# Kernel optimization log

Measured on AMD Instinct MI355X. Metric: run time of the kernel, lower is better.

Reference implementation:

```python
import jax, jax.numpy as jnp
import numpy as np

BATCH, N_BEADS, BEAD_SIZE, N_ATOMS = 32, 16384, 16, 100000
INV_SQRT2 = 0.7071067811865476  # e3nn 'uuu' 1o x 1o -> 1e (irrep_normalization='none') cross-product scale


def _mask_arrays():
    # Deterministic bead->atom mask: bead h places count_h = (h % 16) + 1 atoms.
    counts = np.arange(N_BEADS) % BEAD_SIZE + 1
    mask = np.arange(BEAD_SIZE)[None, :] < counts[:, None]  # (n_beads, bead_size)
    slot_idx = np.nonzero(mask.ravel())[0].astype(np.int32)  # flat positions of True entries, (M,)
    bead_idx = np.repeat(np.arange(N_BEADS), counts).astype(np.int32)  # bead id per placed atom, (M,)
    return slot_idx, bead_idx


def setup_inputs() -> dict:
    slot_idx, bead_idx = _mask_arrays()
    M = slot_idx.shape[0]  # 139264
    rng = np.random.default_rng(0)
    atom_idx = rng.integers(0, N_ATOMS, size=M).astype(np.int32)  # bead2atom_idcs flattened over beads
    key = jax.random.key(0)
    kP, k1, k2, kw, ka, ks = jax.random.split(key, 6)
    return {
        'P': jax.random.normal(kP, (BATCH, N_BEADS, 3), jnp.float32),
        'p1': jax.random.normal(k1, (BATCH, N_BEADS, 3), jnp.float32),
        'p2': jax.random.normal(k2, (BATCH, N_BEADS, 3), jnp.float32),
        'weights': jax.random.normal(kw, (3, N_BEADS, BEAD_SIZE), jnp.float32),
        'angles_polar': jax.random.normal(ka, (M, 1), jnp.float32),
        'scaling': jax.random.normal(ks, (N_ATOMS, 1), jnp.float32),
        'slot_idx': jnp.asarray(slot_idx),
        'atom_idx': jnp.asarray(atom_idx),
        'bead_idx': jnp.asarray(bead_idx),
    }


def _q_mult(q1, q2):
    w1, x1, y1, z1 = jnp.moveaxis(q1, -1, 0)
    w2, x2, y2, z2 = jnp.moveaxis(q2, -1, 0)
    w = w1 * w2 - x1 * x2 - y1 * y2 - z1 * z2
    x = w1 * x2 + x1 * w2 + y1 * z2 - z1 * y2
    y = w1 * y2 + y1 * w2 + z1 * x2 - x1 * z2
    z = w1 * z2 + z1 * w2 + x1 * y2 - y1 * x2
    return jnp.stack((w, x, y, z), -1)


def _qv_mult(q, v):
    q2 = jnp.concatenate([jnp.zeros(v.shape[:-1] + (1,), v.dtype), v], -1)
    q_conj = q * jnp.asarray([1.0, -1.0, -1.0, -1.0], q.dtype)
    return _q_mult(_q_mult(q, q2), q_conj)[..., 1:]


def reference(P, p1, p2, weights, angles_polar, scaling, slot_idx, atom_idx, bead_idx):
    B = P.shape[0]
    # per-bead cross product (e3nn TensorProduct 'uuu' path)
    p12 = jnp.cross(p1, p2) * jnp.asarray(INV_SQRT2, p1.dtype)
    stacked = jnp.stack([p1, p2, p12], axis=1)                      # (B, 3, H, 3)
    rot = jnp.einsum('bihk,ihl->bhlk', stacked, weights)            # (B, H, L, 3)
    rot = rot / jnp.linalg.norm(rot, axis=-1, keepdims=True)
    rot_flat = rot.reshape(B, N_BEADS * BEAD_SIZE, 3)[:, slot_idx]  # (B, M, 3) gather via mask
    # quaternions: real = cos(theta), imag = sin(theta) * axis
    cos_a = jnp.cos(angles_polar)                                   # (M, 1)
    sin_a = jnp.sin(angles_polar)
    q = jnp.concatenate([jnp.broadcast_to(cos_a, (B,) + cos_a.shape), sin_a[None] * rot_flat], -1)  # (B, M, 4)
    v = p1[:, bead_idx]                                             # (B, M, 3) repeat_interleave by counts
    v_rot = _qv_mult(q, v)                                          # (B, M, 3)
    recon = scaling[atom_idx][None] * v_rot + P[:, bead_idx]        # (B, M, 3)
    out = jnp.zeros((B, N_ATOMS, 3), P.dtype).at[:, atom_idx].add(recon)  # scatter-add (overlaps accumulate)
    return out, rot_flat.reshape(-1, 3)
```

## Files before the change

kernel.cpp:

```cpp
#include <hip/hip_runtime.h>
#include <hip/hip_fp16.h>
#include <math.h>

#define BATCH   32
#define N_BEADS 16384
#define BEAD_SIZE 16
#define N_ATOMS 100000
#define INV_SQRT2 0.70710678118654752440f
#define SCAN_BLK 256

__global__ void __launch_bounds__(256)
zero_kernel(int* __restrict__ p, int n)
{
    int i = blockIdx.x * 256 + threadIdx.x;
    if (i < n) p[i] = 0;
}

__global__ void __launch_bounds__(256)
countrec_kernel(const int* __restrict__ atom_idx,
                const int* __restrict__ slot_idx,
                const float* __restrict__ W,
                int* __restrict__ counts,
                float4* __restrict__ rec1, int M)
{
    int m = blockIdx.x * blockDim.x + threadIdx.x;
    if (m >= M) return;
    atomicAdd(&counts[atom_idx[m]], 1);
    int slot = slot_idx[m];
    int h = slot >> 4, l = slot & 15;
    float w0 = W[(0 * N_BEADS + h) * BEAD_SIZE + l];
    float w1 = W[(1 * N_BEADS + h) * BEAD_SIZE + l];
    float w2 = W[(2 * N_BEADS + h) * BEAD_SIZE + l];
    rec1[m] = make_float4(__int_as_float(slot), w0, w1, w2);
}

__global__ void __launch_bounds__(SCAN_BLK)
scan1_kernel(const int* __restrict__ counts, int* __restrict__ off,
             int* __restrict__ bsum, int n)
{
    __shared__ int s[SCAN_BLK];
    int i = blockIdx.x * SCAN_BLK + threadIdx.x;
    int c = (i < n) ? counts[i] : 0;
    s[threadIdx.x] = c;
    __syncthreads();
    int v = c;
    for (int d = 1; d < SCAN_BLK; d <<= 1) {
        int t = (threadIdx.x >= d) ? s[threadIdx.x - d] : 0;
        __syncthreads();
        v += t;
        s[threadIdx.x] = v;
        __syncthreads();
    }
    if (i < n) off[i] = v - c;
    if (threadIdx.x == SCAN_BLK - 1) bsum[blockIdx.x] = v;
}

__global__ void __launch_bounds__(256)
scan3_kernel(int* __restrict__ off, const int* __restrict__ bsum,
             const int* __restrict__ counts,
             int* __restrict__ cursor2, float4* __restrict__ rec_a, int n)
{
    __shared__ int red[256];
    int j = blockIdx.x;
    int partial = 0;
    for (int i = threadIdx.x; i < j; i += 256) partial += bsum[i];
    red[threadIdx.x] = partial;
    __syncthreads();
    for (int d = 128; d > 0; d >>= 1) {
        if ((int)threadIdx.x < d) red[threadIdx.x] += red[threadIdx.x + d];
        __syncthreads();
    }
    int bpref = red[0];
    int i = j * 256 + threadIdx.x;
    if (i >= n) return;
    int o = off[i] + bpref;
    off[i] = o;
    cursor2[i] = 0;
    rec_a[i] = make_float4(__int_as_float(counts[i]), __int_as_float(o),
                           0.f, 0.f);
}

__global__ void __launch_bounds__(256)
fill2_kernel(const int* __restrict__ atom_idx, const int* __restrict__ off,
             const float* __restrict__ ang, const float* __restrict__ scal,
             int* __restrict__ cursor2, int* __restrict__ csr_m,
             float4* __restrict__ recM2, int M)
{
    int m = blockIdx.x * blockDim.x + threadIdx.x;
    if (m >= M) return;
    int a = atom_idx[m];
    int k = atomicAdd(&cursor2[a], 1);
    csr_m[off[a] + k] = m;
    float sa, ca;
    __sincosf(ang[m], &sa, &ca);
    recM2[m] = make_float4(2.f * ca * sa, 2.f * sa * sa, scal[a], 0.f);
}

__global__ void __launch_bounds__(256)
mcontrib_kernel(const float4* __restrict__ rec1,
                const float4* __restrict__ recM2,
                const float* __restrict__ p1,
                const float* __restrict__ p2,
                const float* __restrict__ P,
                float* __restrict__ out_rot,
                uint2* __restrict__ cM16,
                int M)
{
    int bg = blockIdx.y;
    int mbase = blockIdx.x * 256;
    int m = mbase + threadIdx.x;
    int b0 = bg * 4;
    bool act = m < M;
    int mc = act ? m : (M - 1);

    float4 r1 = rec1[mc];
    float4 r2 = recM2[mc];
    int h = __float_as_int(r1.x) >> 4;
    float A = r2.x, Bc = r2.y, s = r2.z;
    size_t hoff = (size_t)h * 3;

    __shared__ float sbuf[768];
    int nm = M - mbase; if (nm > 256) nm = 256;
    int nf = nm * 3;
    int nf4 = nf >> 2;
    int done = nf4 << 2;
    int rem = nf - done;

#pragma unroll
    for (int i = 0; i < 4; ++i) {
        int b = b0 + i;
        const size_t bb = (size_t)b * N_BEADS * 3;
        const float* p1p = p1 + bb + hoff;
        const float* p2p = p2 + bb + hoff;
        const float* Pp  = P  + bb + hoff;
        float a1x = p1p[0], a1y = p1p[1], a1z = p1p[2];
        float a2x = p2p[0], a2y = p2p[1], a2z = p2p[2];

        float cxx = (a1y * a2z - a1z * a2y) * INV_SQRT2;
        float cyy = (a1z * a2x - a1x * a2z) * INV_SQRT2;
        float czz = (a1x * a2y - a1y * a2x) * INV_SQRT2;
        float rx = r1.y * a1x + r1.z * a2x + r1.w * cxx;
        float ry = r1.y * a1y + r1.z * a2y + r1.w * cyy;
        float rz = r1.y * a1z + r1.z * a2z + r1.w * czz;
        float inv = rsqrtf(rx * rx + ry * ry + rz * rz);
        rx *= inv; ry *= inv; rz *= inv;

        __syncthreads();
        sbuf[threadIdx.x * 3 + 0] = rx;
        sbuf[threadIdx.x * 3 + 1] = ry;
        sbuf[threadIdx.x * 3 + 2] = rz;
        __syncthreads();
        {
            size_t base = ((size_t)b * M + mbase) * 3;
            float4* dst = (float4*)(out_rot + base);
            if ((base & 3) == 0) {
                if ((int)threadIdx.x < nf4)
                    dst[threadIdx.x] = ((const float4*)sbuf)[threadIdx.x];
                if ((int)threadIdx.x < rem)
                    out_rot[base + done + threadIdx.x] = sbuf[done + threadIdx.x];
            } else if (act) {
                out_rot[base + threadIdx.x * 3 + 0] = rx;
                out_rot[base + threadIdx.x * 3 + 1] = ry;
                out_rot[base + threadIdx.x * 3 + 2] = rz;
            }
        }

        float ux = ry * a1z - rz * a1y;
        float uy = rz * a1x - rx * a1z;
        float uz = rx * a1y - ry * a1x;
        float wx = ry * uz - rz * uy;
        float wy = rz * ux - rx * uz;
        float wz = rx * uy - ry * ux;
        float ox = s * (a1x + A * ux + Bc * wx) + Pp[0];
        float oy = s * (a1y + A * uy + Bc * wy) + Pp[1];
        float oz = s * (a1z + A * uz + Bc * wz) + Pp[2];

        if (act) {
            union { struct { __half2 lo, hi; } h; uint2 u; } pk;
            pk.h.lo = __floats2half2_rn(ox, oy);
            pk.h.hi = __floats2half2_rn(oz, 0.f);
            cM16[(size_t)b * M + m] = pk.u;
        }
    }
}

__global__ void __launch_bounds__(256)
sum2_kernel(const float4* __restrict__ rec_a,
            const int* __restrict__ csr_m,
            const uint2* __restrict__ cM16,
            float* __restrict__ out_atoms, int M, int abps)
{
    int beta = blockIdx.x;
    int xcd  = beta & 7;
    int j    = beta >> 3;
    int round = j / abps;
    int ablk  = j - round * abps;
    int b = xcd + 8 * round;
    int abase = ablk * 256;
    int a = abase + threadIdx.x;

    float ax = 0.f, ay = 0.f, az = 0.f;
    if (a < N_ATOMS) {
        float4 ra = rec_a[a];
        int cnt = __float_as_int(ra.x);
        int o   = __float_as_int(ra.y);
        const uint2* cb = cM16 + (size_t)b * M;
        for (int k = 0; k < cnt; ++k) {
            int m = csr_m[o + k];
            union { uint2 u; struct { __half2 lo, hi; } h; } pk;
            pk.u = cb[m];
            float2 xy = __half22float2(pk.h.lo);
            float2 zp = __half22float2(pk.h.hi);
            ax += xy.x; ay += xy.y; az += zp.x;
        }
    }
    __shared__ float sbuf[768];
    sbuf[threadIdx.x * 3 + 0] = ax;
    sbuf[threadIdx.x * 3 + 1] = ay;
    sbuf[threadIdx.x * 3 + 2] = az;
    __syncthreads();

    int na = N_ATOMS - abase; if (na > 256) na = 256;
    int nf = na * 3;
    size_t base = ((size_t)b * N_ATOMS + abase) * 3;
    int nf4 = nf >> 2;
    float4* dst = (float4*)(out_atoms + base);
    if ((int)threadIdx.x < nf4)
        dst[threadIdx.x] = ((const float4*)sbuf)[threadIdx.x];
    int done = nf4 << 2;
    int rem = nf - done;
    if ((int)threadIdx.x < rem)
        out_atoms[base + done + threadIdx.x] = sbuf[done + threadIdx.x];
}

__global__ void __launch_bounds__(256)
backmap_fallback(const float* __restrict__ P, const float* __restrict__ p1,
                 const float* __restrict__ p2, const float* __restrict__ W,
                 const float* __restrict__ ang, const float* __restrict__ scal,
                 const int* __restrict__ slot_idx, const int* __restrict__ atom_idx,
                 float* __restrict__ out_atoms, float* __restrict__ out_rot, int M)
{
    int t = blockIdx.x * blockDim.x + threadIdx.x;
    if (t >= BATCH * M) return;
    int b = t / M; int m = t - b * M;
    int slot = slot_idx[m]; int h = slot >> 4; int l = slot & 15;
    int atom = atom_idx[m];
    const float* p1p = p1 + ((size_t)b * N_BEADS + h) * 3;
    const float* p2p = p2 + ((size_t)b * N_BEADS + h) * 3;
    float a1x = p1p[0], a1y = p1p[1], a1z = p1p[2];
    float a2x = p2p[0], a2y = p2p[1], a2z = p2p[2];
    float cx = (a1y * a2z - a1z * a2y) * INV_SQRT2;
    float cy = (a1z * a2x - a1x * a2z) * INV_SQRT2;
    float cz = (a1x * a2y - a1y * a2x) * INV_SQRT2;
    float w0 = W[(0 * N_BEADS + h) * BEAD_SIZE + l];
    float w1 = W[(1 * N_BEADS + h) * BEAD_SIZE + l];
    float w2 = W[(2 * N_BEADS + h) * BEAD_SIZE + l];
    float rx = w0 * a1x + w1 * a2x + w2 * cx;
    float ry = w0 * a1y + w1 * a2y + w2 * cy;
    float rz = w0 * a1z + w1 * a2z + w2 * cz;
    float inv = rsqrtf(rx * rx + ry * ry + rz * rz);
    rx *= inv; ry *= inv; rz *= inv;
    float* ro = out_rot + (size_t)t * 3;
    ro[0] = rx; ro[1] = ry; ro[2] = rz;
    float sa, ca; __sincosf(ang[m], &sa, &ca);
    float A = 2.f * ca * sa, Bc = 2.f * sa * sa;
    float ux = ry * a1z - rz * a1y;
    float uy = rz * a1x - rx * a1z;
    float uz = rx * a1y - ry * a1x;
    float wx = ry * uz - rz * uy;
    float wy = rz * ux - rx * uz;
    float wz = rx * uy - ry * ux;
    float s = scal[atom];
    const float* Pp = P + ((size_t)b * N_BEADS + h) * 3;
    float* op = out_atoms + ((size_t)b * N_ATOMS + atom) * 3;
    atomicAdd(op + 0, s * (a1x + A * ux + Bc * wx) + Pp[0]);
    atomicAdd(op + 1, s * (a1y + A * uy + Bc * wy) + Pp[1]);
    atomicAdd(op + 2, s * (a1z + A * uz + Bc * wz) + Pp[2]);
}

extern "C" void kernel_launch(void* const* d_in, const int* in_sizes, int n_in,
                              void* d_out, int out_size, void* d_ws, size_t ws_size,
                              hipStream_t stream) {
    const float* P    = (const float*)d_in[0];
    const float* p1   = (const float*)d_in[1];
    const float* p2   = (const float*)d_in[2];
    const float* W    = (const float*)d_in[3];
    const float* ang  = (const float*)d_in[4];
    const float* scal = (const float*)d_in[5];
    const int* slot_idx = (const int*)d_in[6];
    const int* atom_idx = (const int*)d_in[7];

    int M = in_sizes[6];
    float* out_atoms = (float*)d_out;
    float* out_rot   = out_atoms + (size_t)BATCH * N_ATOMS * 3;

    int nblk   = (N_ATOMS + SCAN_BLK - 1) / SCAN_BLK;
    int nchunk = (M + 255) / 256;

    size_t intpre = (size_t)N_ATOMS * 4 * 3 + 512 * 4;
    size_t need   = intpre + (size_t)M * 16 * 2 + (size_t)N_ATOMS * 16
                  + (size_t)M * 4 + (size_t)BATCH * M * 8;

    if (ws_size >= need) {
        int* counts  = (int*)d_ws;
        int* off     = counts + N_ATOMS;
        int* cursor2 = off + N_ATOMS;
        int* bsum    = cursor2 + N_ATOMS;
        float4* rec1  = (float4*)((char*)d_ws + intpre);
        float4* recM2 = rec1 + M;
        float4* rec_a = recM2 + M;
        int*    csr_m = (int*)(rec_a + N_ATOMS);
        uint2*  cM16  = (uint2*)(csr_m + M);

        zero_kernel<<<nblk, 256, 0, stream>>>(counts, N_ATOMS);
        countrec_kernel<<<nchunk, 256, 0, stream>>>(
            atom_idx, slot_idx, W, counts, rec1, M);
        scan1_kernel<<<nblk, SCAN_BLK, 0, stream>>>(counts, off, bsum, N_ATOMS);
        scan3_kernel<<<nblk, 256, 0, stream>>>(off, bsum, counts,
                                               cursor2, rec_a, N_ATOMS);
        fill2_kernel<<<nchunk, 256, 0, stream>>>(
            atom_idx, off, ang, scal, cursor2, csr_m, recM2, M);

        dim3 gm(nchunk, 8);
        mcontrib_kernel<<<gm, 256, 0, stream>>>(
            rec1, recM2, p1, p2, P, out_rot, cM16, M);

        int abps = (N_ATOMS + 255) / 256;
        sum2_kernel<<<abps * BATCH, 256, 0, stream>>>(
            rec_a, csr_m, cM16, out_atoms, M, abps);
        return;
    }

    hipMemsetAsync(out_atoms, 0, (size_t)BATCH * N_ATOMS * 3 * sizeof(float), stream);
    int total = BATCH * M;
    backmap_fallback<<<(total + 255) / 256, 256, 0, stream>>>(
        P, p1, p2, W, ang, scal, slot_idx, atom_idx,
        out_atoms, out_rot, M);
}
```

Before: 91.72 us.

## Stage per-block bead vectors in LDS and batch rotation stores after compute

The mcontrib kernel now loads each block's contiguous range of bead vectors (p1, p2, P for four batches) into shared memory with cooperative coalesced reads, replacing repeated strided per-thread global loads. It falls back to global loads if a bead lies outside the staged range. The rot outputs for all four batches are buffered in shared memory, so the two barriers per batch iteration are replaced by one barrier and a final coalesced store pass. This uses more shared memory and adds a staging barrier, which may reduce occupancy.

```diff
diff --git a/kernel.cpp b/kernel.cpp
--- a/kernel.cpp
+++ b/kernel.cpp
@@ -8,6 +8,7 @@
 #define N_ATOMS 100000
 #define INV_SQRT2 0.70710678118654752440f
 #define SCAN_BLK 256
+#define NH 64
 
 __global__ void __launch_bounds__(256)
 zero_kernel(int* __restrict__ p, int n)
@@ -108,7 +109,8 @@
 {
     int bg = blockIdx.y;
     int mbase = blockIdx.x * 256;
-    int m = mbase + threadIdx.x;
+    int tid = threadIdx.x;
+    int m = mbase + tid;
     int b0 = bg * 4;
     bool act = m < M;
     int mc = act ? m : (M - 1);
@@ -117,24 +119,49 @@
     float4 r2 = recM2[mc];
     int h = __float_as_int(r1.x) >> 4;
     float A = r2.x, Bc = r2.y, s = r2.z;
-    size_t hoff = (size_t)h * 3;
-
-    __shared__ float sbuf[768];
-    int nm = M - mbase; if (nm > 256) nm = 256;
-    int nf = nm * 3;
-    int nf4 = nf >> 2;
-    int done = nf4 << 2;
-    int rem = nf - done;
+
+    __shared__ float sbead[4][3][NH * 3];
+    __shared__ float srot[4][768];
+    __shared__ int   shh[2];
+
+    if (tid == 0)   shh[0] = h;
+    if (tid == 255) shh[1] = h;
+    __syncthreads();
+    int h0 = shh[0];
+    int nh = shh[1] - h0 + 1;
+    if (nh > NH) nh = NH;
+
+    int per_a = nh * 3;
+    int per_b = 3 * per_a;
+    int totd  = 4 * per_b;
+    for (int idx = tid; idx < totd; idx += 256) {
+        int i = idx / per_b;
+        int r = idx - i * per_b;
+        int a = r / per_a;
+        int c = r - a * per_a;
+        const float* src = (a == 0) ? p1 : (a == 1) ? p2 : P;
+        sbead[i][a][c] = src[((size_t)(b0 + i) * N_BEADS + h0) * 3 + c];
+    }
+    __syncthreads();
+
+    int dh = h - h0;
+    bool inlds = (dh >= 0) & (dh < nh);
+    int d3 = dh * 3;
 
 #pragma unroll
     for (int i = 0; i < 4; ++i) {
         int b = b0 + i;
-        const size_t bb = (size_t)b * N_BEADS * 3;
-        const float* p1p = p1 + bb + hoff;
-        const float* p2p = p2 + bb + hoff;
-        const float* Pp  = P  + bb + hoff;
-        float a1x = p1p[0], a1y = p1p[1], a1z = p1p[2];
-        float a2x = p2p[0], a2y = p2p[1], a2z = p2p[2];
+        float a1x, a1y, a1z, a2x, a2y, a2z, Px, Py, Pz;
+        if (inlds) {
+            a1x = sbead[i][0][d3];  a1y = sbead[i][0][d3 + 1]; a1z = sbead[i][0][d3 + 2];
+            a2x = sbead[i][1][d3];  a2y = sbead[i][1][d3 + 1]; a2z = sbead[i][1][d3 + 2];
+            Px  = sbead[i][2][d3];  Py  = sbead[i][2][d3 + 1]; Pz  = sbead[i][2][d3 + 2];
+        } else {
+            const size_t bb = ((size_t)b * N_BEADS + h) * 3;
+            a1x = p1[bb]; a1y = p1[bb + 1]; a1z = p1[bb + 2];
+            a2x = p2[bb]; a2y = p2[bb + 1]; a2z = p2[bb + 2];
+            Px  = P[bb];  Py  = P[bb + 1];  Pz  = P[bb + 2];
+        }
 
         float cxx = (a1y * a2z - a1z * a2y) * INV_SQRT2;
         float cyy = (a1z * a2x - a1x * a2z) * INV_SQRT2;
@@ -145,25 +172,9 @@
         float inv = rsqrtf(rx * rx + ry * ry + rz * rz);
         rx *= inv; ry *= inv; rz *= inv;
 
-        __syncthreads();
-        sbuf[threadIdx.x * 3 + 0] = rx;
-        sbuf[threadIdx.x * 3 + 1] = ry;
-        sbuf[threadIdx.x * 3 + 2] = rz;
-        __syncthreads();
-        {
-            size_t base = ((size_t)b * M + mbase) * 3;
-            float4* dst = (float4*)(out_rot + base);
-            if ((base & 3) == 0) {
-                if ((int)threadIdx.x < nf4)
-                    dst[threadIdx.x] = ((const float4*)sbuf)[threadIdx.x];
-                if ((int)threadIdx.x < rem)
-                    out_rot[base + done + threadIdx.x] = sbuf[done + threadIdx.x];
-            } else if (act) {
-                out_rot[base + threadIdx.x * 3 + 0] = rx;
-                out_rot[base + threadIdx.x * 3 + 1] = ry;
-                out_rot[base + threadIdx.x * 3 + 2] = rz;
-            }
-        }
+        srot[i][tid * 3 + 0] = rx;
+        srot[i][tid * 3 + 1] = ry;
+        srot[i][tid * 3 + 2] = rz;
 
         float ux = ry * a1z - rz * a1y;
         float uy = rz * a1x - rx * a1z;
@@ -171,15 +182,37 @@
         float wx = ry * uz - rz * uy;
         float wy = rz * ux - rx * uz;
         float wz = rx * uy - ry * ux;
-        float ox = s * (a1x + A * ux + Bc * wx) + Pp[0];
-        float oy = s * (a1y + A * uy + Bc * wy) + Pp[1];
-        float oz = s * (a1z + A * uz + Bc * wz) + Pp[2];
+        float ox = s * (a1x + A * ux + Bc * wx) + Px;
+        float oy = s * (a1y + A * uy + Bc * wy) + Py;
+        float oz = s * (a1z + A * uz + Bc * wz) + Pz;
 
         if (act) {
-            union { struct { __half2 lo, hi; } h; uint2 u; } pk;
-            pk.h.lo = __floats2half2_rn(ox, oy);
-            pk.h.hi = __floats2half2_rn(oz, 0.f);
+            union { struct { __half2 lo, hi; } hh; uint2 u; } pk;
+            pk.hh.lo = __floats2half2_rn(ox, oy);
+            pk.hh.hi = __floats2half2_rn(oz, 0.f);
             cM16[(size_t)b * M + m] = pk.u;
+        }
+    }
+    __syncthreads();
+
+    int nm = M - mbase; if (nm > 256) nm = 256;
+    int nf = nm * 3;
+    int nf4 = nf >> 2;
+    int done = nf4 << 2;
+    int rem = nf - done;
+#pragma unroll
+    for (int i = 0; i < 4; ++i) {
+        size_t base = ((size_t)(b0 + i) * M + mbase) * 3;
+        if ((base & 3) == 0) {
+            float4* dst = (float4*)(out_rot + base);
+            if (tid < nf4)
+                dst[tid] = ((const float4*)srot[i])[tid];
+            if (tid < rem)
+                out_rot[base + done + tid] = srot[i][done + tid];
+        } else if (act) {
+            out_rot[base + tid * 3 + 0] = srot[i][tid * 3 + 0];
+            out_rot[base + tid * 3 + 1] = srot[i][tid * 3 + 1];
+            out_rot[base + tid * 3 + 2] = srot[i][tid * 3 + 2];
         }
     }
 }
@@ -207,10 +240,10 @@
         const uint2* cb = cM16 + (size_t)b * M;
         for (int k = 0; k < cnt; ++k) {
             int m = csr_m[o + k];
-            union { uint2 u; struct { __half2 lo, hi; } h; } pk;
+            union { uint2 u; struct { __half2 lo, hi; } hh; } pk;
             pk.u = cb[m];
-            float2 xy = __half22float2(pk.h.lo);
-            float2 zp = __half22float2(pk.h.hi);
+            float2 xy = __half22float2(pk.hh.lo);
+            float2 zp = __half22float2(pk.hh.hi);
             ax += xy.x; ay += xy.y; az += zp.x;
         }
     }
```

After: 94.54 us. +3.1%, slower.
